# Optimization experiments

Measured on AMD Instinct MI355X. Metric: run time of the kernel, lower is better.

## Reference

```python
import jax, jax.numpy as jnp
import numpy as np

NB = 50  # nb_steps
IN_D = 64
HID = 128
B = 256


def _cc_weights(nb):
    # Faithful port of UMNN compute_cc_weights (Clenshaw-Curtis quadrature)
    lam = np.arange(0, nb + 1).reshape(-1, 1).astype(np.float64)
    lam = np.cos((lam @ lam.T) * np.pi / nb)
    lam[:, 0] = 0.5
    lam[:, -1] = 0.5 * lam[:, -1]
    lam = lam * 2.0 / nb
    W = np.arange(0, nb + 1).reshape(-1, 1).astype(np.float64)
    W[np.arange(1, nb + 1, 2)] = 0
    W = 2.0 / (1.0 - W ** 2)
    W[0] = 1
    W[np.arange(1, nb + 1, 2)] = 0
    cc = (lam.T @ W)[:, 0].astype(np.float32)              # [nb+1]
    steps = np.cos(np.arange(0, nb + 1) * np.pi / nb).astype(np.float32)  # [nb+1]
    return jnp.asarray(cc), jnp.asarray(steps)


def setup_inputs() -> dict:
    key = jax.random.key(0)
    ks = jax.random.split(key, 16)
    d = {}
    d["x"] = jax.random.normal(ks[0], (B, 1), dtype=jnp.float32)
    d["h"] = jax.random.normal(ks[1], (B, IN_D - 1), dtype=jnp.float32)

    def lin(kw, kb, fan_in, fan_out):
        s = 1.0 / np.sqrt(fan_in)
        w = jax.random.uniform(kw, (fan_in, fan_out), jnp.float32, -s, s)
        b = jax.random.uniform(kb, (fan_out,), jnp.float32, -s, s)
        return w, b

    # Integrand MLP: in_d -> 128 -> 128 -> 1
    d["iw0"], d["ib0"] = lin(ks[2], ks[3], IN_D, HID)
    d["iw1"], d["ib1"] = lin(ks[4], ks[5], HID, HID)
    d["iw2"], d["ib2"] = lin(ks[6], ks[7], HID, 1)
    # Outer net: (in_d-1) -> 128 -> 128 -> 2
    d["nw0"], d["nb0"] = lin(ks[8], ks[9], IN_D - 1, HID)
    d["nw1"], d["nb1"] = lin(ks[10], ks[11], HID, HID)
    d["nw2"], d["nb2"] = lin(ks[12], ks[13], HID, 2)
    return d


def reference(x, h, iw0, ib0, iw1, ib1, iw2, ib2, nw0, nb0, nw1, nb1, nw2, nb2):
    cc, steps = _cc_weights(NB)  # [S1], [S1]
    S1 = NB + 1
    b = x.shape[0]

    # ----- outer quadrature: integral over t in [0, x] -----
    # t[b, i] = 0 + (x - 0) * (steps[i] + 1) / 2
    t = x[:, None, :] * (steps[None, :, None] + 1.0) / 2.0          # [B, S1, 1]

    # ----- inner UMNN: integral over s in [t, xmax], xmax = max(t) + 10 -----
    xmax = jnp.max(t) + 10.0
    s = t[:, :, None, :] + (xmax - t)[:, :, None, :] * (steps[None, None, :, None] + 1.0) / 2.0  # [B,S1,S1,1]

    hb = jnp.broadcast_to(h[:, None, None, :], (b, S1, S1, h.shape[1]))
    inp = jnp.concatenate([s, hb], axis=-1)                         # [B,S1,S1,in_d]

    # PostiveIntegrandNN: Lin-ReLU-Lin-ReLU-Lin-ELU, then + 1.0
    a = jax.nn.relu(inp @ iw0 + ib0)
    a = jax.nn.relu(a @ iw1 + ib1)
    f = jax.nn.elu(a @ iw2 + ib2) + 1.0                              # [B,S1,S1,1]

    # inner Clenshaw-Curtis reduction: z * (xT - x0) / 2
    inner = jnp.sum(f * cc[None, None, :, None], axis=2) * (xmax - t) / 2.0   # [B,S1,1]

    # outer reduction: integral from 0 to x
    outer = jnp.sum(inner * cc[None, :, None], axis=1) * x / 2.0    # [B,1]

    # outer dense net on h -> offset / scaling
    o = jax.nn.relu(h @ nw0 + nb0)
    o = jax.nn.relu(o @ nw1 + nb1)
    o = o @ nw2 + nb2                                               # [B,2]
    offset = o[:, 0:1]
    scaling = jnp.exp(o[:, 1:2])
    return scaling * outer + offset
```

## Files before the change

### kernel.cpp

```cpp
#include <hip/hip_runtime.h>
#include <math.h>

#define NBQ 50
#define S1 51
#define NPTS 2601
#define IN_D 64
#define HID 128
#define BSZ 256
#define NCHUNK 4
#define NUMAX 41

typedef __bf16 bf16x8 __attribute__((ext_vector_type(8)));
typedef float  f32x4  __attribute__((ext_vector_type(4)));

#define WS_CC     0
#define WS_STEPS  64
#define WS_XMAX   128
#define WS_BASE   256
#define WS_SCAL   33024
#define WS_OFF    33280
#define WS_PART   33536
#define WS_W1BF   41728

__global__ void k_prep(const float* __restrict__ x, const float* __restrict__ h,
                       const float* __restrict__ iw0, const float* __restrict__ ib0,
                       const float* __restrict__ iw1,
                       const float* __restrict__ nw0, const float* __restrict__ nb0,
                       const float* __restrict__ nw1, const float* __restrict__ nb1,
                       const float* __restrict__ nw2, const float* __restrict__ nb2,
                       float* __restrict__ ws) {
    int blk = blockIdx.x;
    int tid = threadIdx.x;

    if (blk < 64) {
        int idx  = blk * 256 + tid;
        int e    = idx & 7;
        int lane = (idx >> 3) & 63;
        int fk   = idx >> 9;
        int kk   = fk & 3;
        int nt   = fk >> 2;
        int k = kk * 32 + (lane >> 4) * 8 + e;
        int n = nt * 16 + (lane & 15);
        __bf16* w1bf = (__bf16*)(ws + WS_W1BF);
        w1bf[idx] = (__bf16)iw1[k * HID + n];
        return;
    }

    __shared__ float s_steps[S1];
    __shared__ float s_red[4];
    __shared__ float s_h[IN_D - 1];
    __shared__ float s_o0[HID];
    __shared__ float s_part[4];

    if (blk == 64) {
        int t = tid;
        if (t < S1) {
            double st = cos((double)t * M_PI / (double)NBQ);
            s_steps[t] = (float)st;
            ws[WS_STEPS + t] = (float)st;
            double acc = 0.0;
            for (int i = 0; i <= NBQ; ++i) {
                double Wi;
                if (i == 0)       Wi = 1.0;
                else if (i & 1)   Wi = 0.0;
                else              Wi = 2.0 / (1.0 - (double)i * (double)i);
                double lam;
                if (t == 0)  lam = 0.5;
                else         lam = cos((double)i * (double)t * M_PI / (double)NBQ);
                if (t == NBQ) lam *= 0.5;
                lam *= 2.0 / (double)NBQ;
                acc += lam * Wi;
            }
            ws[WS_CC + t] = (float)acc;
        }
        __syncthreads();
        float xb = x[t];
        float m = -1e30f;
        for (int i = 0; i < S1; ++i)
            m = fmaxf(m, xb * (s_steps[i] + 1.0f) * 0.5f);
        for (int off = 32; off > 0; off >>= 1)
            m = fmaxf(m, __shfl_down(m, off));
        if ((t & 63) == 0) s_red[t >> 6] = m;
        __syncthreads();
        if (t == 0) {
            float mm = fmaxf(fmaxf(s_red[0], s_red[1]), fmaxf(s_red[2], s_red[3]));
            ws[WS_XMAX] = mm + 10.0f;
        }
        return;
    }

    int b = blk - 65;
    int n = tid;
    bool act = (n < HID);
    if (act && n < IN_D - 1) s_h[n] = h[b * (IN_D - 1) + n];
    __syncthreads();
    float o1 = 0.0f;
    if (act) {
        float aB0 = ib0[n], aB1 = 0.f, aB2 = 0.f, aB3 = 0.f;
        float a00 = nb0[n], a01 = 0.f, a02 = 0.f, a03 = 0.f;
        int d = 0;
        for (; d + 4 <= IN_D - 1; d += 4) {
            float h0 = s_h[d], h1 = s_h[d + 1], h2 = s_h[d + 2], h3 = s_h[d + 3];
            aB0 = fmaf(h0, iw0[(1 + d) * HID + n], aB0);
            aB1 = fmaf(h1, iw0[(2 + d) * HID + n], aB1);
            aB2 = fmaf(h2, iw0[(3 + d) * HID + n], aB2);
            aB3 = fmaf(h3, iw0[(4 + d) * HID + n], aB3);
            a00 = fmaf(h0, nw0[(d)     * HID + n], a00);
            a01 = fmaf(h1, nw0[(d + 1) * HID + n], a01);
            a02 = fmaf(h2, nw0[(d + 2) * HID + n], a02);
            a03 = fmaf(h3, nw0[(d + 3) * HID + n], a03);
        }
        for (; d < IN_D - 1; ++d) {
            float hv = s_h[d];
            aB0 = fmaf(hv, iw0[(1 + d) * HID + n], aB0);
            a00 = fmaf(hv, nw0[d * HID + n], a00);
        }
        ws[WS_BASE + b * HID + n] = (aB0 + aB1) + (aB2 + aB3);
        s_o0[n] = fmaxf((a00 + a01) + (a02 + a03), 0.0f);
    }
    __syncthreads();
    if (act) {
        float a0 = nb1[n], a1 = 0.f, a2 = 0.f, a3 = 0.f;
        for (int m = 0; m < HID; m += 4) {
            a0 = fmaf(s_o0[m],     nw1[(m)     * HID + n], a0);
            a1 = fmaf(s_o0[m + 1], nw1[(m + 1) * HID + n], a1);
            a2 = fmaf(s_o0[m + 2], nw1[(m + 2) * HID + n], a2);
            a3 = fmaf(s_o0[m + 3], nw1[(m + 3) * HID + n], a3);
        }
        o1 = fmaxf((a0 + a1) + (a2 + a3), 0.0f);
    }
    float p0 = act ? o1 * nw2[n * 2 + 0] : 0.0f;
    float p1 = act ? o1 * nw2[n * 2 + 1] : 0.0f;
    for (int off = 32; off > 0; off >>= 1) {
        p0 += __shfl_down(p0, off);
        p1 += __shfl_down(p1, off);
    }
    int lane = tid & 63, w = tid >> 6;
    if (lane == 0 && w < 2) { s_part[w * 2] = p0; s_part[w * 2 + 1] = p1; }
    __syncthreads();
    if (tid == 0) {
        ws[WS_OFF + b]  = s_part[0] + s_part[2] + nb2[0];
        ws[WS_SCAL + b] = expf(s_part[1] + s_part[3] + nb2[1]);
    }
}

__global__ __launch_bounds__(256, 4) void k3_mfma(
        const float* __restrict__ x,
        const float* __restrict__ iw0,
        const float* __restrict__ ib1,
        const float* __restrict__ iw2,
        const float* __restrict__ ib2,
        float* __restrict__ ws) {
    __shared__ bf16x8 bfr_lds[4][4][64];
    __shared__ float zlds[4][NUMAX][17];
    __shared__ float s_tbl[NUMAX][16];
    __shared__ float w_tbl[NUMAX][16];

    int blk  = blockIdx.x;
    int b    = blk >> 2;
    int c    = blk & 3;
    int tid  = threadIdx.x;
    int wave = tid >> 6;
    int lane = tid & 63;
    int col  = lane & 15;
    int g    = lane >> 4;

    float xmax = ws[WS_XMAX];
    float xb   = x[b];
    float b2   = ib2[0];

    int NU = (c < 3) ? 41 : 40;
    int G  = (NU + 3) >> 2;

    for (int e = tid; e < NU * 16; e += 256) {
        int u  = e >> 4;
        int cl = e & 15;
        int p  = (c + 4 * u) * 16 + cl;
        int pc = (p < NPTS) ? p : (NPTS - 1);
        int i  = (int)(((unsigned)pc * 10281u) >> 19);
        int j  = pc - i * 51;
        float sti = ws[WS_STEPS + i];
        float stj = ws[WS_STEPS + j];
        float ti  = xb * (sti + 1.0f) * 0.5f;
        float w   = xmax - ti;
        s_tbl[u][cl] = fmaf(w, (stj + 1.0f) * 0.5f, ti);
        w_tbl[u][cl] = (p < NPTS) ? ws[WS_CC + i] * ws[WS_CC + j] * w : 0.0f;
    }

    const bf16x8* w1f = (const bf16x8*)(ws + WS_W1BF);
    bf16x8 Af[2][4];
#pragma unroll
    for (int nt = 0; nt < 2; ++nt) {
        int NT = wave * 2 + nt;
#pragma unroll
        for (int kk = 0; kk < 4; ++kk)
            Af[nt][kk] = w1f[(NT * 4 + kk) * 64 + lane];
    }

    const float* basep = ws + WS_BASE + b * HID;
    int m0 = wave * 32 + g * 8;
    f32x4 w0a = *(const f32x4*)(iw0 + m0);
    f32x4 w0b = *(const f32x4*)(iw0 + m0 + 4);
    f32x4 bsa = *(const f32x4*)(basep + m0);
    f32x4 bsb = *(const f32x4*)(basep + m0 + 4);

    f32x4 accInit[2], iw2v[2];
#pragma unroll
    for (int nt = 0; nt < 2; ++nt) {
        int n0 = (wave * 2 + nt) * 16 + g * 4;
        accInit[nt] = *(const f32x4*)(ib1 + n0);
        iw2v[nt]    = *(const f32x4*)(iw2 + n0);
    }

    __syncthreads();

    for (int grp = 0; grp < G; ++grp) {
        int ubase = grp * 4;
#pragma unroll
        for (int t = 0; t < 4; ++t) {
            int u = ubase + t;
            if (u < NU) {
                float s = s_tbl[u][col];
                bf16x8 bfr;
#pragma unroll
                for (int e = 0; e < 4; ++e) {
                    bfr[e]     = (__bf16)fmaxf(fmaf(s, w0a[e], bsa[e]), 0.0f);
                    bfr[4 + e] = (__bf16)fmaxf(fmaf(s, w0b[e], bsb[e]), 0.0f);
                }
                bfr_lds[t][wave][lane] = bfr;
            }
        }
        __syncthreads();
#pragma unroll
        for (int t = 0; t < 4; ++t) {
            int u = ubase + t;
            if (u < NU) {
                bf16x8 f0 = bfr_lds[t][0][lane];
                bf16x8 f1 = bfr_lds[t][1][lane];
                bf16x8 f2 = bfr_lds[t][2][lane];
                bf16x8 f3 = bfr_lds[t][3][lane];
                __builtin_amdgcn_s_setprio(1);
                f32x4 a0 = __builtin_amdgcn_mfma_f32_16x16x32_bf16(Af[0][0], f0, accInit[0], 0, 0, 0);
                f32x4 a1 = __builtin_amdgcn_mfma_f32_16x16x32_bf16(Af[1][0], f0, accInit[1], 0, 0, 0);
                a0 = __builtin_amdgcn_mfma_f32_16x16x32_bf16(Af[0][1], f1, a0, 0, 0, 0);
                a1 = __builtin_amdgcn_mfma_f32_16x16x32_bf16(Af[1][1], f1, a1, 0, 0, 0);
                a0 = __builtin_amdgcn_mfma_f32_16x16x32_bf16(Af[0][2], f2, a0, 0, 0, 0);
                a1 = __builtin_amdgcn_mfma_f32_16x16x32_bf16(Af[1][2], f2, a1, 0, 0, 0);
                a0 = __builtin_amdgcn_mfma_f32_16x16x32_bf16(Af[0][3], f3, a0, 0, 0, 0);
                a1 = __builtin_amdgcn_mfma_f32_16x16x32_bf16(Af[1][3], f3, a1, 0, 0, 0);
                __builtin_amdgcn_s_setprio(0);

                float za = 0.f, zb = 0.f;
#pragma unroll
                for (int q = 0; q < 4; ++q) {
                    za = fmaf(fmaxf(a0[q], 0.0f), iw2v[0][q], za);
                    zb = fmaf(fmaxf(a1[q], 0.0f), iw2v[1][q], zb);
                }
                float z = za + zb;
                z += __shfl_xor(z, 16);
                z += __shfl_xor(z, 32);
                if (lane < 16) zlds[wave][u][lane] = z;
            }
        }
        __syncthreads();
    }

    float vsum = 0.0f;
    int npass = (NU + 15) >> 4;
    for (int pass = 0; pass < npass; ++pass) {
        int u = pass * 16 + wave * 4 + g;
        if (u < NU) {
            float z = zlds[0][u][col] + zlds[1][u][col]
                    + zlds[2][u][col] + zlds[3][u][col] + b2;
            float f = (z > 0.0f) ? (z + 1.0f) : __expf(z);
            vsum += w_tbl[u][col] * f;
        }
    }
#pragma unroll
    for (int off = 1; off < 64; off <<= 1)
        vsum += __shfl_xor(vsum, off);
    if (lane == 0)
        ws[WS_PART + blk * 4 + wave] = vsum * 0.5f;
}

__global__ void k4_final(const float* __restrict__ x, const float* __restrict__ ws,
                         float* __restrict__ out) {
    int b = threadIdx.x;
    float sum = 0.0f;
#pragma unroll
    for (int c = 0; c < 16; ++c) sum += ws[WS_PART + b * 16 + c];
    out[b] = ws[WS_SCAL + b] * sum * x[b] * 0.5f + ws[WS_OFF + b];
}

extern "C" void kernel_launch(void* const* d_in, const int* in_sizes, int n_in,
                              void* d_out, int out_size, void* d_ws, size_t ws_size,
                              hipStream_t stream) {
    const float* x   = (const float*)d_in[0];
    const float* h   = (const float*)d_in[1];
    const float* iw0 = (const float*)d_in[2];
    const float* ib0 = (const float*)d_in[3];
    const float* iw1 = (const float*)d_in[4];
    const float* ib1 = (const float*)d_in[5];
    const float* iw2 = (const float*)d_in[6];
    const float* ib2 = (const float*)d_in[7];
    const float* nw0 = (const float*)d_in[8];
    const float* nb0 = (const float*)d_in[9];
    const float* nw1 = (const float*)d_in[10];
    const float* nb1 = (const float*)d_in[11];
    const float* nw2 = (const float*)d_in[12];
    const float* nb2 = (const float*)d_in[13];
    float* ws  = (float*)d_ws;
    float* out = (float*)d_out;

    hipLaunchKernelGGL(k_prep, dim3(64 + 1 + BSZ), dim3(256), 0, stream,
                       x, h, iw0, ib0, iw1, nw0, nb0, nw1, nb1, nw2, nb2, ws);
    hipLaunchKernelGGL(k3_mfma, dim3(BSZ * NCHUNK), dim3(256), 0, stream,
                       x, iw0, ib1, iw2, ib2, ws);
    hipLaunchKernelGGL(k4_final, dim3(1), dim3(BSZ), 0, stream, x, ws, out);
}
```

Baseline: 49.91 us.

## Move outer dense net from prep kernel into main MFMA kernel as extra blocks

```diff
diff --git a/kernel.cpp b/kernel.cpp
--- a/kernel.cpp
+++ b/kernel.cpp
@@ -9,6 +9,8 @@
 #define BSZ 256
 #define NCHUNK 4
 #define NUMAX 41
+#define NMAIN 1024
+#define NNET  128
 
 typedef __bf16 bf16x8 __attribute__((ext_vector_type(8)));
 typedef float  f32x4  __attribute__((ext_vector_type(4)));
@@ -25,9 +27,6 @@
 __global__ void k_prep(const float* __restrict__ x, const float* __restrict__ h,
                        const float* __restrict__ iw0, const float* __restrict__ ib0,
                        const float* __restrict__ iw1,
-                       const float* __restrict__ nw0, const float* __restrict__ nb0,
-                       const float* __restrict__ nw1, const float* __restrict__ nb1,
-                       const float* __restrict__ nw2, const float* __restrict__ nb2,
                        float* __restrict__ ws) {
     int blk = blockIdx.x;
     int tid = threadIdx.x;
@@ -48,9 +47,7 @@
 
     __shared__ float s_steps[S1];
     __shared__ float s_red[4];
-    __shared__ float s_h[IN_D - 1];
-    __shared__ float s_o0[HID];
-    __shared__ float s_part[4];
+    __shared__ float s_h2[2][64];
 
     if (blk == 64) {
         int t = tid;
@@ -89,59 +86,22 @@
         return;
     }
 
-    int b = blk - 65;
-    int n = tid;
-    bool act = (n < HID);
-    if (act && n < IN_D - 1) s_h[n] = h[b * (IN_D - 1) + n];
+    int sub = tid >> 7;
+    int n   = tid & 127;
+    int b   = (blk - 65) * 2 + sub;
+    if (n < IN_D - 1) s_h2[sub][n] = h[b * (IN_D - 1) + n];
     __syncthreads();
-    float o1 = 0.0f;
-    if (act) {
-        float aB0 = ib0[n], aB1 = 0.f, aB2 = 0.f, aB3 = 0.f;
-        float a00 = nb0[n], a01 = 0.f, a02 = 0.f, a03 = 0.f;
-        int d = 0;
-        for (; d + 4 <= IN_D - 1; d += 4) {
-            float h0 = s_h[d], h1 = s_h[d + 1], h2 = s_h[d + 2], h3 = s_h[d + 3];
-            aB0 = fmaf(h0, iw0[(1 + d) * HID + n], aB0);
-            aB1 = fmaf(h1, iw0[(2 + d) * HID + n], aB1);
-            aB2 = fmaf(h2, iw0[(3 + d) * HID + n], aB2);
-            aB3 = fmaf(h3, iw0[(4 + d) * HID + n], aB3);
-            a00 = fmaf(h0, nw0[(d)     * HID + n], a00);
-            a01 = fmaf(h1, nw0[(d + 1) * HID + n], a01);
-            a02 = fmaf(h2, nw0[(d + 2) * HID + n], a02);
-            a03 = fmaf(h3, nw0[(d + 3) * HID + n], a03);
-        }
-        for (; d < IN_D - 1; ++d) {
-            float hv = s_h[d];
-            aB0 = fmaf(hv, iw0[(1 + d) * HID + n], aB0);
-            a00 = fmaf(hv, nw0[d * HID + n], a00);
-        }
-        ws[WS_BASE + b * HID + n] = (aB0 + aB1) + (aB2 + aB3);
-        s_o0[n] = fmaxf((a00 + a01) + (a02 + a03), 0.0f);
-    }
-    __syncthreads();
-    if (act) {
-        float a0 = nb1[n], a1 = 0.f, a2 = 0.f, a3 = 0.f;
-        for (int m = 0; m < HID; m += 4) {
-            a0 = fmaf(s_o0[m],     nw1[(m)     * HID + n], a0);
-            a1 = fmaf(s_o0[m + 1], nw1[(m + 1) * HID + n], a1);
-            a2 = fmaf(s_o0[m + 2], nw1[(m + 2) * HID + n], a2);
-            a3 = fmaf(s_o0[m + 3], nw1[(m + 3) * HID + n], a3);
-        }
-        o1 = fmaxf((a0 + a1) + (a2 + a3), 0.0f);
-    }
-    float p0 = act ? o1 * nw2[n * 2 + 0] : 0.0f;
-    float p1 = act ? o1 * nw2[n * 2 + 1] : 0.0f;
-    for (int off = 32; off > 0; off >>= 1) {
-        p0 += __shfl_down(p0, off);
-        p1 += __shfl_down(p1, off);
-    }
-    int lane = tid & 63, w = tid >> 6;
-    if (lane == 0 && w < 2) { s_part[w * 2] = p0; s_part[w * 2 + 1] = p1; }
-    __syncthreads();
-    if (tid == 0) {
-        ws[WS_OFF + b]  = s_part[0] + s_part[2] + nb2[0];
-        ws[WS_SCAL + b] = expf(s_part[1] + s_part[3] + nb2[1]);
-    }
+    float aB0 = ib0[n], aB1 = 0.f, aB2 = 0.f, aB3 = 0.f;
+    int d = 0;
+    for (; d + 4 <= IN_D - 1; d += 4) {
+        aB0 = fmaf(s_h2[sub][d],     iw0[(1 + d) * HID + n], aB0);
+        aB1 = fmaf(s_h2[sub][d + 1], iw0[(2 + d) * HID + n], aB1);
+        aB2 = fmaf(s_h2[sub][d + 2], iw0[(3 + d) * HID + n], aB2);
+        aB3 = fmaf(s_h2[sub][d + 3], iw0[(4 + d) * HID + n], aB3);
+    }
+    for (; d < IN_D - 1; ++d)
+        aB0 = fmaf(s_h2[sub][d], iw0[(1 + d) * HID + n], aB0);
+    ws[WS_BASE + b * HID + n] = (aB0 + aB1) + (aB2 + aB3);
 }
 
 __global__ __launch_bounds__(256, 4) void k3_mfma(
@@ -150,6 +110,10 @@
         const float* __restrict__ ib1,
         const float* __restrict__ iw2,
         const float* __restrict__ ib2,
+        const float* __restrict__ h,
+        const float* __restrict__ nw0, const float* __restrict__ nb0,
+        const float* __restrict__ nw1, const float* __restrict__ nb1,
+        const float* __restrict__ nw2, const float* __restrict__ nb2,
         float* __restrict__ ws) {
     __shared__ bf16x8 bfr_lds[4][4][64];
     __shared__ float zlds[4][NUMAX][17];
@@ -157,9 +121,57 @@
     __shared__ float w_tbl[NUMAX][16];
 
     int blk  = blockIdx.x;
+    int tid  = threadIdx.x;
+
+    if (blk >= NMAIN) {
+        float* scratch = (float*)bfr_lds;
+        float* s_h  = scratch;
+        float* s_o0 = scratch + 128;
+        float* s_pp = scratch + 384;
+        int sub = tid >> 7;
+        int n   = tid & 127;
+        int wig = (tid >> 6) & 1;
+        int lane = tid & 63;
+        int b   = (blk - NMAIN) * 2 + sub;
+        if (n < IN_D - 1) s_h[sub * 64 + n] = h[b * (IN_D - 1) + n];
+        __syncthreads();
+        float a00 = nb0[n], a01 = 0.f, a02 = 0.f, a03 = 0.f;
+        int d = 0;
+        for (; d + 4 <= IN_D - 1; d += 4) {
+            a00 = fmaf(s_h[sub * 64 + d],     nw0[(d)     * HID + n], a00);
+            a01 = fmaf(s_h[sub * 64 + d + 1], nw0[(d + 1) * HID + n], a01);
+            a02 = fmaf(s_h[sub * 64 + d + 2], nw0[(d + 2) * HID + n], a02);
+            a03 = fmaf(s_h[sub * 64 + d + 3], nw0[(d + 3) * HID + n], a03);
+        }
+        for (; d < IN_D - 1; ++d)
+            a00 = fmaf(s_h[sub * 64 + d], nw0[d * HID + n], a00);
+        s_o0[sub * 128 + n] = fmaxf((a00 + a01) + (a02 + a03), 0.0f);
+        __syncthreads();
+        float a0 = nb1[n], a1 = 0.f, a2 = 0.f, a3 = 0.f;
+        for (int m = 0; m < HID; m += 4) {
+            a0 = fmaf(s_o0[sub * 128 + m],     nw1[(m)     * HID + n], a0);
+            a1 = fmaf(s_o0[sub * 128 + m + 1], nw1[(m + 1) * HID + n], a1);
+            a2 = fmaf(s_o0[sub * 128 + m + 2], nw1[(m + 2) * HID + n], a2);
+            a3 = fmaf(s_o0[sub * 128 + m + 3], nw1[(m + 3) * HID + n], a3);
+        }
+        float o1 = fmaxf((a0 + a1) + (a2 + a3), 0.0f);
+        float p0 = o1 * nw2[n * 2 + 0];
+        float p1 = o1 * nw2[n * 2 + 1];
+        for (int off = 32; off > 0; off >>= 1) {
+            p0 += __shfl_down(p0, off);
+            p1 += __shfl_down(p1, off);
+        }
+        if (lane == 0) { s_pp[sub * 4 + wig * 2] = p0; s_pp[sub * 4 + wig * 2 + 1] = p1; }
+        __syncthreads();
+        if (n == 0) {
+            ws[WS_OFF + b]  = s_pp[sub * 4 + 0] + s_pp[sub * 4 + 2] + nb2[0];
+            ws[WS_SCAL + b] = expf(s_pp[sub * 4 + 1] + s_pp[sub * 4 + 3] + nb2[1]);
+        }
+        return;
+    }
+
     int b    = blk >> 2;
     int c    = blk & 3;
-    int tid  = threadIdx.x;
     int wave = tid >> 6;
     int lane = tid & 63;
     int col  = lane & 15;
@@ -312,9 +324,9 @@
     float* ws  = (float*)d_ws;
     float* out = (float*)d_out;
 
-    hipLaunchKernelGGL(k_prep, dim3(64 + 1 + BSZ), dim3(256), 0, stream,
-                       x, h, iw0, ib0, iw1, nw0, nb0, nw1, nb1, nw2, nb2, ws);
-    hipLaunchKernelGGL(k3_mfma, dim3(BSZ * NCHUNK), dim3(256), 0, stream,
-                       x, iw0, ib1, iw2, ib2, ws);
+    hipLaunchKernelGGL(k_prep, dim3(64 + 1 + 128), dim3(256), 0, stream,
+                       x, h, iw0, ib0, iw1, ws);
+    hipLaunchKernelGGL(k3_mfma, dim3(NMAIN + NNET), dim3(256), 0, stream,
+                       x, iw0, ib1, iw2, ib2, h, nw0, nb0, nw1, nb1, nw2, nb2, ws);
     hipLaunchKernelGGL(k4_final, dim3(1), dim3(BSZ), 0, stream, x, ws, out);
 }
```

After: 50.46 us. About the same (+1.1%).
